# Performance work log

Measured on AMD Instinct MI355X. Metric: run time of the kernel, lower is better.

Reference implementation:

```python
import jax, jax.numpy as jnp
import numpy as np

EPS = 1e-5
K = 7            # involution kernel size
GC = 16          # group_channels (involution default)
RED = 4          # reduction ratio (involution default)


def _bn(x, g, b, m, v):
    # eval-mode BatchNorm2d over channel dim of NCHW
    scale = g / jnp.sqrt(v + EPS)
    return x * scale[None, :, None, None] + (b - m * scale)[None, :, None, None]


def setup_inputs() -> dict:
    key = jax.random.key(0)
    ks = jax.random.split(key, 24)
    C_in, C_out = 64, 128
    B, H, W = 4, 96, 96
    G = C_in // GC          # 4 involution groups
    Cr = C_in // RED        # 16 reduced channels

    def bn_params(k, c):
        k1, k2, k3, k4 = jax.random.split(k, 4)
        return (jax.random.uniform(k1, (c,)) + 0.5,          # gamma
                jax.random.normal(k2, (c,)) * 0.1,            # beta
                jax.random.normal(k3, (c,)) * 0.1,            # running mean
                jax.random.uniform(k4, (c,)) + 0.5)           # running var

    g_r, b_r, m_r, v_r = bn_params(ks[1], Cr)
    g_i, b_i, m_i, v_i = bn_params(ks[2], C_in)
    g_c, b_c, m_c, v_c = bn_params(ks[3], C_out)
    g_m, b_m, m_m, v_m = bn_params(ks[4], C_out)

    return {
        "x": jax.random.normal(ks[0], (B, C_in, H, W), dtype=jnp.float32),
        "w_reduce": jax.random.normal(ks[5], (Cr, C_in), dtype=jnp.float32) * 0.1,
        "g_r": g_r, "b_r": b_r, "m_r": m_r, "v_r": v_r,
        "w_span": jax.random.normal(ks[6], (K * K * G, Cr), dtype=jnp.float32) * 0.1,
        "b_span": jax.random.normal(ks[7], (K * K * G,), dtype=jnp.float32) * 0.1,
        "g_i": g_i, "b_i": b_i, "m_i": m_i, "v_i": v_i,
        "w_conv": jax.random.normal(ks[8], (C_out, C_in), dtype=jnp.float32) * 0.1,
        "g_c": g_c, "b_c": b_c, "m_c": m_c, "v_c": v_c,
        "w_map": jax.random.normal(ks[9], (C_out, C_in), dtype=jnp.float32) * 0.1,
        "b_map": jax.random.normal(ks[10], (C_out,), dtype=jnp.float32) * 0.1,
        "g_m": g_m, "b_m": b_m, "m_m": m_m, "v_m": v_m,
    }


def reference(x, w_reduce, g_r, b_r, m_r, v_r, w_span, b_span,
              g_i, b_i, m_i, v_i, w_conv, g_c, b_c, m_c, v_c,
              w_map, b_map, g_m, b_m, m_m, v_m):
    B, C, H, W = x.shape
    G = C // GC
    pad = (K - 1) // 2

    # --- Involution: dynamic per-pixel kernels ---
    t = jax.nn.relu(_bn(jnp.einsum('rc,bchw->brhw', w_reduce, x), g_r, b_r, m_r, v_r))
    kern = jnp.einsum('or,brhw->bohw', w_span, t) + b_span[None, :, None, None]
    kern = kern.reshape(B, G, 1, K * K, H, W)  # [B,G,1,KK,H,W]

    xp = jnp.pad(x, ((0, 0), (0, 0), (pad, pad), (pad, pad)))
    # unfold in torch (C, kh, kw) order: C slowest -> stack over kernel offsets
    patches = jnp.stack([xp[:, :, i:i + H, j:j + W]
                         for i in range(K) for j in range(K)], axis=2)  # [B,C,KK,H,W]
    patches = patches.reshape(B, G, GC, K * K, H, W)
    inv = (kern * patches).sum(axis=3).reshape(B, C, H, W)

    # --- BN + GELU, 1x1 conv + BN, mapping branch, residual + GELU ---
    x1 = jax.nn.gelu(_bn(inv, g_i, b_i, m_i, v_i), approximate=False)
    x1 = _bn(jnp.einsum('oc,bchw->bohw', w_conv, x1), g_c, b_c, m_c, v_c)
    xm = _bn(jnp.einsum('oc,bchw->bohw', w_map, x) + b_map[None, :, None, None],
             g_m, b_m, m_m, v_m)
    return jax.nn.gelu(x1 + xm, approximate=False)
```

## Files before the change

### kernel.cpp

```cpp
#include <hip/hip_runtime.h>
#include <hip/hip_bf16.h>
#include <math.h>

typedef __hip_bfloat16 bf16;
typedef __attribute__((ext_vector_type(8))) short v8s;
typedef __attribute__((ext_vector_type(4))) float v4f;

#define HD 96
#define WD 96
#define HW 9216
#define BATCH 4

#define OFF_WR    0
#define OFF_CR    1024
#define OFF_WSP   1040
#define OFF_BSP   4176
#define OFF_SI    4372
#define OFF_CI    4436
#define OFF_BIAS  4500
#define WFRAG_BYTE 18512
#define X1_BYTE   51328

__device__ __forceinline__ float geluf(float v) {
    return 0.5f * v * (1.0f + erff(v * 0.7071067811865475f));
}

__global__ __launch_bounds__(256) void k_fold(
    const float* __restrict__ wred,
    const float* __restrict__ gr, const float* __restrict__ br,
    const float* __restrict__ mr, const float* __restrict__ vr,
    const float* __restrict__ wspan, const float* __restrict__ bspan,
    const float* __restrict__ gi, const float* __restrict__ bi,
    const float* __restrict__ mi, const float* __restrict__ vi,
    const float* __restrict__ wconv,
    const float* __restrict__ gc, const float* __restrict__ bc,
    const float* __restrict__ mc, const float* __restrict__ vc,
    const float* __restrict__ wmap, const float* __restrict__ bmap,
    const float* __restrict__ gm, const float* __restrict__ bm,
    const float* __restrict__ mmn, const float* __restrict__ vm,
    float* __restrict__ wsf, bf16* __restrict__ wfrag)
{
    const int gt = blockIdx.x * 256 + threadIdx.x;

    if (gt < 1024) {
        int r = gt >> 6;
        float sr = gr[r] * rsqrtf(vr[r] + 1e-5f);
        wsf[OFF_WR + gt] = sr * wred[gt];
    }
    if (gt < 16) {
        float sr = gr[gt] * rsqrtf(vr[gt] + 1e-5f);
        wsf[OFF_CR + gt] = br[gt] - mr[gt] * sr;
    }
    if (gt < 3136) wsf[OFF_WSP + gt] = wspan[gt];
    if (gt < 196)  wsf[OFF_BSP + gt] = bspan[gt];
    if (gt < 64) {
        float si = gi[gt] * rsqrtf(vi[gt] + 1e-5f);
        wsf[OFF_SI + gt] = si;
        wsf[OFF_CI + gt] = bi[gt] - mi[gt] * si;
    }
    if (gt < 128) {
        float sc = gc[gt] * rsqrtf(vc[gt] + 1e-5f);
        float sm = gm[gt] * rsqrtf(vm[gt] + 1e-5f);
        wsf[OFF_BIAS + gt] = (bc[gt] - mc[gt] * sc)
                           + sm * bmap[gt]
                           + (bm[gt] - mmn[gt] * sm);
    }
    {
        int j    = gt & 7;
        int lane = (gt >> 3) & 63;
        int ks   = (gt >> 9) & 3;
        int mt   = gt >> 11;
        int m = mt * 16 + (lane & 15);
        int k = ks * 32 + (lane >> 4) * 8 + j;
        float v;
        if (k < 64) {
            float sc = gc[m] * rsqrtf(vc[m] + 1e-5f);
            v = sc * wconv[m * 64 + k];
        } else {
            float sm = gm[m] * rsqrtf(vm[m] + 1e-5f);
            v = sm * wmap[m * 64 + (k - 64)];
        }
        wfrag[gt] = __float2bfloat16(v);
    }
}

__global__ __launch_bounds__(256) void k_inv2(
    const float* __restrict__ x, const float* __restrict__ wsf,
    bf16* __restrict__ x1)
{
    __shared__ float xs4[3136];
    __shared__ float ks[49 * 64];
    __shared__ float ts[64 * 17];

    const int tid = threadIdx.x;
    const int bz  = blockIdx.z;
    const int b   = bz >> 2, g = bz & 3;
    const int ty  = blockIdx.y * 8, tx = blockIdx.x * 8;

    const float* xb = x + (size_t)b * 64 * HW;

    for (int it = tid; it < 784; it += 256) {
        int qc = it / 196, pos = it % 196;
        int py = pos / 14, px = pos % 14;
        int gy = ty + py - 3, gx = tx + px - 3;
        v4f v = (v4f){0.f, 0.f, 0.f, 0.f};
        if (gy >= 0 && gy < HD && gx >= 0 && gx < WD) {
            const float* pp = xb + (size_t)(g * 16 + qc * 4) * HW + gy * WD + gx;
            v[0] = pp[0]; v[1] = pp[HW]; v[2] = pp[2 * HW]; v[3] = pp[3 * HW];
        }
        *(v4f*)&xs4[it * 4] = v;
    }

    const int p  = tid & 63;
    const int u  = __builtin_amdgcn_readfirstlane(tid >> 6);
    const int py0 = p >> 3, px0 = p & 7;
    const int hw  = (ty + py0) * WD + (tx + px0);

    float t4[4];
    #pragma unroll
    for (int r = 0; r < 4; ++r) t4[r] = wsf[OFF_CR + u * 4 + r];
    #pragma unroll 4
    for (int c = 0; c < 64; ++c) {
        float xc = xb[(size_t)c * HW + hw];
        #pragma unroll
        for (int r = 0; r < 4; ++r)
            t4[r] += wsf[OFF_WR + (u * 4 + r) * 64 + c] * xc;
    }
    #pragma unroll
    for (int r = 0; r < 4; ++r) ts[p * 17 + u * 4 + r] = fmaxf(t4[r], 0.0f);
    __syncthreads();

    float tr[16];
    #pragma unroll
    for (int r = 0; r < 16; ++r) tr[r] = ts[p * 17 + r];

    for (int kk = u; kk < 49; kk += 4) {
        int row = g * 49 + kk;
        float kv = wsf[OFF_BSP + row];
        #pragma unroll
        for (int r = 0; r < 16; ++r) kv += wsf[OFF_WSP + row * 16 + r] * tr[r];
        ks[kk * 64 + p] = kv;
    }
    __syncthreads();

    float acc[4] = {0.f, 0.f, 0.f, 0.f};
    #pragma unroll 1
    for (int i = 0; i < 7; ++i) {
        const int rowb = (py0 + i) * 14 + px0;
        #pragma unroll
        for (int j = 0; j < 7; ++j) {
            float kv = ks[(i * 7 + j) * 64 + p];
            v4f xv = *(const v4f*)&xs4[(u * 196 + rowb + j) * 4];
            acc[0] += kv * xv[0];
            acc[1] += kv * xv[1];
            acc[2] += kv * xv[2];
            acc[3] += kv * xv[3];
        }
    }

    const int c0 = g * 16 + u * 4;
    bf16* x1b = x1 + ((size_t)b * 64 + c0) * HW + hw;
    #pragma unroll
    for (int ci = 0; ci < 4; ++ci) {
        float v = acc[ci] * wsf[OFF_SI + c0 + ci] + wsf[OFF_CI + c0 + ci];
        x1b[(size_t)ci * HW] = __float2bfloat16(geluf(v));
    }
}

#define ZPAD 136
__global__ __launch_bounds__(256) void k_out(
    const float* __restrict__ x, const bf16* __restrict__ x1,
    const float* __restrict__ wsf, const bf16* __restrict__ wfrag,
    float* __restrict__ out)
{
    __shared__ bf16 zl[64 * ZPAD];

    const int tid  = threadIdx.x;
    const int lane = tid & 63;
    const int cw   = tid >> 6;
    const int tile = blockIdx.x * 64;
    const int b    = tile / HW;
    const int hw0  = tile % HW;

    const bf16*  x1b = x1 + (size_t)b * 64 * HW + hw0;
    const float* xb  = x  + (size_t)b * 64 * HW + hw0;

    #pragma unroll
    for (int r = 0; r < 32; ++r) {
        int ch = r * 4 + cw;
        bf16 v;
        if (ch < 64) v = x1b[(size_t)ch * HW + lane];
        else         v = __float2bfloat16(xb[(size_t)(ch - 64) * HW + lane]);
        zl[lane * ZPAD + ch] = v;
    }
    __syncthreads();

    const int n    = lane & 15;
    const int quad = lane >> 4;
    const int pxl  = cw * 16 + n;

    v4f acc[8];
    #pragma unroll
    for (int mt = 0; mt < 8; ++mt) acc[mt] = (v4f){0.f, 0.f, 0.f, 0.f};

    const v8s* wf = (const v8s*)wfrag;
    #pragma unroll
    for (int ks = 0; ks < 4; ++ks) {
        v8s bfrag = *(const v8s*)&zl[pxl * ZPAD + ks * 32 + quad * 8];
        #pragma unroll
        for (int mt = 0; mt < 8; ++mt) {
            v8s afrag = wf[(mt * 4 + ks) * 64 + lane];
            acc[mt] = __builtin_amdgcn_mfma_f32_16x16x32_bf16(afrag, bfrag, acc[mt], 0, 0, 0);
        }
    }

    const int hw = hw0 + pxl;
    #pragma unroll
    for (int mt = 0; mt < 8; ++mt) {
        int m0 = mt * 16 + quad * 4;
        v4f bs = *(const v4f*)&wsf[OFF_BIAS + m0];
        #pragma unroll
        for (int reg = 0; reg < 4; ++reg) {
            float v = acc[mt][reg] + bs[reg];
            out[((size_t)(b * 128 + m0 + reg)) * HW + hw] = geluf(v);
        }
    }
}

extern "C" void kernel_launch(void* const* d_in, const int* in_sizes, int n_in,
                              void* d_out, int out_size, void* d_ws, size_t ws_size,
                              hipStream_t stream)
{
    const float* x     = (const float*)d_in[0];
    const float* wred  = (const float*)d_in[1];
    const float* gr    = (const float*)d_in[2];
    const float* br    = (const float*)d_in[3];
    const float* mr    = (const float*)d_in[4];
    const float* vr    = (const float*)d_in[5];
    const float* wspan = (const float*)d_in[6];
    const float* bspan = (const float*)d_in[7];
    const float* gi    = (const float*)d_in[8];
    const float* bi    = (const float*)d_in[9];
    const float* mi    = (const float*)d_in[10];
    const float* vi    = (const float*)d_in[11];
    const float* wconv = (const float*)d_in[12];
    const float* gc    = (const float*)d_in[13];
    const float* bc    = (const float*)d_in[14];
    const float* mc    = (const float*)d_in[15];
    const float* vc    = (const float*)d_in[16];
    const float* wmap  = (const float*)d_in[17];
    const float* bmap  = (const float*)d_in[18];
    const float* gm    = (const float*)d_in[19];
    const float* bm    = (const float*)d_in[20];
    const float* mmn   = (const float*)d_in[21];
    const float* vm    = (const float*)d_in[22];

    float* wsf   = (float*)d_ws;
    bf16*  wfrag = (bf16*)((char*)d_ws + WFRAG_BYTE);
    bf16*  x1    = (bf16*)((char*)d_ws + X1_BYTE);
    float* out   = (float*)d_out;

    hipLaunchKernelGGL(k_fold, dim3(64), dim3(256), 0, stream,
                       wred, gr, br, mr, vr, wspan, bspan, gi, bi, mi, vi,
                       wconv, gc, bc, mc, vc, wmap, bmap, gm, bm, mmn, vm,
                       wsf, wfrag);
    hipLaunchKernelGGL(k_inv2, dim3(12, 12, 16), dim3(256), 0, stream, x, wsf, x1);
    hipLaunchKernelGGL(k_out, dim3((BATCH * HW) / 64), dim3(256), 0, stream,
                       x, x1, wsf, wfrag, out);
}
```

Measured before the change: 160.0 us.

## Write pixel-major bf16 activations and raw x in involution kernel, drop LDS transpose

The involution kernel now writes its GELU output and the bf16-converted center x values into one pixel-major [B*HW,128] buffer, each thread storing 4 contiguous channels. The output GEMM kernel then loads its MFMA B fragments straight from global memory and no longer needs a shared-memory transpose, a re-read of fp32 x, or a barrier. In exchange the stores from the involution kernel are short 8-byte writes strided by 256 bytes per pixel, which may coalesce poorly.

Measured after the change: 159.2 us. No clear change (-0.5%).

```diff
diff --git a/kernel.cpp b/kernel.cpp
--- a/kernel.cpp
+++ b/kernel.cpp
@@ -4,6 +4,7 @@
 
 typedef __hip_bfloat16 bf16;
 typedef __attribute__((ext_vector_type(8))) short v8s;
+typedef __attribute__((ext_vector_type(4))) short v4s;
 typedef __attribute__((ext_vector_type(4))) float v4f;
 
 #define HD 96
@@ -19,7 +20,7 @@
 #define OFF_CI    4436
 #define OFF_BIAS  4500
 #define WFRAG_BYTE 18512
-#define X1_BYTE   51328
+#define ZT_BYTE   51328
 
 __device__ __forceinline__ float geluf(float v) {
     return 0.5f * v * (1.0f + erff(v * 0.7071067811865475f));
@@ -86,7 +87,7 @@
 
 __global__ __launch_bounds__(256) void k_inv2(
     const float* __restrict__ x, const float* __restrict__ wsf,
-    bf16* __restrict__ x1)
+    bf16* __restrict__ zt)
 {
     __shared__ float xs4[3136];
     __shared__ float ks[49 * 64];
@@ -159,62 +160,58 @@
     }
 
     const int c0 = g * 16 + u * 4;
-    bf16* x1b = x1 + ((size_t)b * 64 + c0) * HW + hw;
+    bf16* ztr = zt + ((size_t)b * HW + hw) * 128;
+
+    v4s pk1;
     #pragma unroll
     for (int ci = 0; ci < 4; ++ci) {
         float v = acc[ci] * wsf[OFF_SI + c0 + ci] + wsf[OFF_CI + c0 + ci];
-        x1b[(size_t)ci * HW] = __float2bfloat16(geluf(v));
-    }
-}
-
-#define ZPAD 136
-__global__ __launch_bounds__(256) void k_out(
-    const float* __restrict__ x, const bf16* __restrict__ x1,
-    const float* __restrict__ wsf, const bf16* __restrict__ wfrag,
-    float* __restrict__ out)
-{
-    __shared__ bf16 zl[64 * ZPAD];
-
+        pk1[ci] = (short)__bfloat16_as_ushort(__float2bfloat16(geluf(v)));
+    }
+    *(v4s*)&ztr[c0] = pk1;
+
+    const int center = (py0 + 3) * 14 + (px0 + 3);
+    v4f xc = *(const v4f*)&xs4[(u * 196 + center) * 4];
+    v4s pk2;
+    #pragma unroll
+    for (int ci = 0; ci < 4; ++ci)
+        pk2[ci] = (short)__bfloat16_as_ushort(__float2bfloat16(xc[ci]));
+    *(v4s*)&ztr[64 + c0] = pk2;
+}
+
+__global__ __launch_bounds__(256) void k_out2(
+    const bf16* __restrict__ zt, const float* __restrict__ wsf,
+    const bf16* __restrict__ wfrag, float* __restrict__ out)
+{
     const int tid  = threadIdx.x;
     const int lane = tid & 63;
-    const int cw   = tid >> 6;
-    const int tile = blockIdx.x * 64;
-    const int b    = tile / HW;
-    const int hw0  = tile % HW;
-
-    const bf16*  x1b = x1 + (size_t)b * 64 * HW + hw0;
-    const float* xb  = x  + (size_t)b * 64 * HW + hw0;
-
-    #pragma unroll
-    for (int r = 0; r < 32; ++r) {
-        int ch = r * 4 + cw;
-        bf16 v;
-        if (ch < 64) v = x1b[(size_t)ch * HW + lane];
-        else         v = __float2bfloat16(xb[(size_t)(ch - 64) * HW + lane]);
-        zl[lane * ZPAD + ch] = v;
-    }
-    __syncthreads();
-
+    const int wv   = tid >> 6;
     const int n    = lane & 15;
     const int quad = lane >> 4;
-    const int pxl  = cw * 16 + n;
-
+
+    const int pxg = blockIdx.x * 64 + wv * 16 + n;
+    const int b   = pxg / HW;
+    const int hw  = pxg % HW;
+
+    const v8s* zb = (const v8s*)(zt + (size_t)pxg * 128);
+    v8s bfr[4];
+    #pragma unroll
+    for (int ks = 0; ks < 4; ++ks) bfr[ks] = zb[ks * 4 + quad];
+
+    const v8s* wf = (const v8s*)wfrag;
     v4f acc[8];
     #pragma unroll
     for (int mt = 0; mt < 8; ++mt) acc[mt] = (v4f){0.f, 0.f, 0.f, 0.f};
 
-    const v8s* wf = (const v8s*)wfrag;
     #pragma unroll
     for (int ks = 0; ks < 4; ++ks) {
-        v8s bfrag = *(const v8s*)&zl[pxl * ZPAD + ks * 32 + quad * 8];
         #pragma unroll
         for (int mt = 0; mt < 8; ++mt) {
             v8s afrag = wf[(mt * 4 + ks) * 64 + lane];
-            acc[mt] = __builtin_amdgcn_mfma_f32_16x16x32_bf16(afrag, bfrag, acc[mt], 0, 0, 0);
-        }
-    }
-
-    const int hw = hw0 + pxl;
+            acc[mt] = __builtin_amdgcn_mfma_f32_16x16x32_bf16(afrag, bfr[ks], acc[mt], 0, 0, 0);
+        }
+    }
+
     #pragma unroll
     for (int mt = 0; mt < 8; ++mt) {
         int m0 = mt * 16 + quad * 4;
@@ -257,14 +254,14 @@
 
     float* wsf   = (float*)d_ws;
     bf16*  wfrag = (bf16*)((char*)d_ws + WFRAG_BYTE);
-    bf16*  x1    = (bf16*)((char*)d_ws + X1_BYTE);
+    bf16*  zt    = (bf16*)((char*)d_ws + ZT_BYTE);
     float* out   = (float*)d_out;
 
     hipLaunchKernelGGL(k_fold, dim3(64), dim3(256), 0, stream,
                        wred, gr, br, mr, vr, wspan, bspan, gi, bi, mi, vi,
                        wconv, gc, bc, mc, vc, wmap, bmap, gm, bm, mmn, vm,
                        wsf, wfrag);
-    hipLaunchKernelGGL(k_inv2, dim3(12, 12, 16), dim3(256), 0, stream, x, wsf, x1);
-    hipLaunchKernelGGL(k_out, dim3((BATCH * HW) / 64), dim3(256), 0, stream,
-                       x, x1, wsf, wfrag, out);
-}
+    hipLaunchKernelGGL(k_inv2, dim3(12, 12, 16), dim3(256), 0, stream, x, wsf, zt);
+    hipLaunchKernelGGL(k_out2, dim3((BATCH * HW) / 64), dim3(256), 0, stream,
+                       zt, wsf, wfrag, out);
+}
```
